# Kernel tuning notes

Hardware: AMD Instinct MI355X
Metric: run time of the kernel (lower is better)

The kernel has to match this reference:

```python
import jax, jax.numpy as jnp
import numpy as np

B, T, C = 4, 2048, 1024
H = 16
D = C // H  # head_dim = 64


def setup_inputs() -> dict:
    key = jax.random.key(0)
    ks = jax.random.split(key, 9)
    s = 1.0 / np.sqrt(C)
    return {
        "x": jax.random.normal(ks[0], (B, T, C), dtype=jnp.float32),
        "Wk": jax.random.uniform(ks[1], (C, C), jnp.float32, -s, s),
        "bk": jax.random.uniform(ks[2], (C,), jnp.float32, -s, s),
        "Wq": jax.random.uniform(ks[3], (C, C), jnp.float32, -s, s),
        "bq": jax.random.uniform(ks[4], (C,), jnp.float32, -s, s),
        "Wv": jax.random.uniform(ks[5], (C, C), jnp.float32, -s, s),
        "bv": jax.random.uniform(ks[6], (C,), jnp.float32, -s, s),
        "Wp": jax.random.uniform(ks[7], (C, C), jnp.float32, -s, s),
        "bp": jax.random.uniform(ks[8], (C,), jnp.float32, -s, s),
    }


def reference(x, Wk, bk, Wq, bq, Wv, bv, Wp, bp):
    # projections -> (B, H, T, D)
    def split_heads(y):
        return y.reshape(B, T, H, D).transpose(0, 2, 1, 3)

    k = split_heads(x @ Wk.T + bk)
    q = split_heads(x @ Wq.T + bq)
    v = split_heads(x @ Wv.T + bv)

    att = jnp.einsum("bhtd,bhsd->bhts", q, k) / np.sqrt(D).astype(np.float32)
    causal = jnp.tril(jnp.ones((T, T), dtype=bool))
    att = jnp.where(causal, att, -jnp.inf)
    att = jax.nn.softmax(att, axis=-1)

    y = jnp.einsum("bhts,bhsd->bhtd", att, v)  # (B,H,T,D)
    y = y.transpose(0, 2, 1, 3).reshape(B, T, C)
    return y @ Wp.T + bp
```

## Files before the change

kernel.cpp:

```cpp
#include <hip/hip_runtime.h>
#include <hip/hip_bf16.h>

typedef unsigned short u16;
typedef unsigned int u32;
typedef short short8 __attribute__((ext_vector_type(8)));
typedef short short4v __attribute__((ext_vector_type(4)));
typedef float f32x4 __attribute__((ext_vector_type(4)));

#define MFMA16(a, b, c) __builtin_amdgcn_mfma_f32_16x16x32_bf16((a), (b), (c), 0, 0, 0)

constexpr int kB = 4, kT = 2048, kC = 1024, kH = 16, kD = 64;
constexpr int kBT = kB * kT;
constexpr long kQKV = (long)kB * kH * kT * kD;
constexpr float kSC = 0.125f * 1.4426950408889634f;

__device__ inline u16 f2bf(float f) {
    __hip_bfloat16 h = __float2bfloat16(f);
    return *reinterpret_cast<u16*>(&h);
}
__device__ inline u32 pkbf_trunc(float lo, float hi) {
    u32 a = __builtin_bit_cast(u32, lo);
    u32 b = __builtin_bit_cast(u32, hi);
    return (b & 0xFFFF0000u) | (a >> 16);
}
__device__ inline u32 pkbf_rne(float lo, float hi) {
    return ((u32)f2bf(hi) << 16) | (u32)f2bf(lo);
}

__device__ inline void cp16(const u16* g, u16* l) {
    __builtin_amdgcn_global_load_lds(
        (const __attribute__((address_space(1))) unsigned int*)g,
        (__attribute__((address_space(3))) unsigned int*)l, 16, 0, 0);
}

__global__ __launch_bounds__(256) void cast_kernel(
    const float* __restrict__ x,  const float* __restrict__ Wk,
    const float* __restrict__ Wq, const float* __restrict__ Wv,
    const float* __restrict__ Wp,
    u16* __restrict__ xb, u16* __restrict__ wkb, u16* __restrict__ wqb,
    u16* __restrict__ wvb, u16* __restrict__ wpb)
{
    const long id = (long)blockIdx.x * 256 + threadIdx.x;
    const float* src;
    u16* dst;
    long off;
    if (id < 2097152) {
        src = x; dst = xb; off = id;
    } else {
        const long w = (id - 2097152) >> 18;
        off = (id - 2097152) & 262143;
        src = (w == 0) ? Wk : (w == 1) ? Wq : (w == 2) ? Wv : Wp;
        dst = (w == 0) ? wkb : (w == 1) ? wqb : (w == 2) ? wvb : wpb;
    }
    f32x4 v = *(const f32x4*)&src[off * 4];
    short4v s = {(short)f2bf(v[0]), (short)f2bf(v[1]),
                 (short)f2bf(v[2]), (short)f2bf(v[3])};
    *(short4v*)&dst[off * 4] = s;
}

__global__ __launch_bounds__(256) void qkv_gemm_bf16(
    const u16* __restrict__ xb,
    const u16* __restrict__ wkb, const u16* __restrict__ wqb,
    const u16* __restrict__ wvb,
    const float* __restrict__ bk, const float* __restrict__ bq,
    const float* __restrict__ bv,
    u16* __restrict__ kw, u16* __restrict__ qw, u16* __restrict__ vw)
{
    __shared__ u16 As[128 * 32];
    __shared__ u16 Bs[128 * 32];
    const int tid = threadIdx.x;
    const int lane = tid & 63;
    const int wid = tid >> 6;
    const int l15 = lane & 15;
    const int quad = lane >> 4;
    const int m0 = blockIdx.x * 128;
    const int n0 = blockIdx.y * 128;
    const int z = blockIdx.z;

    const u16* W = (z == 0) ? wkb : (z == 1) ? wqb : wvb;
    const float* bias = (z == 0) ? bk : (z == 1) ? bq : bv;

    f32x4 zero = {0.f, 0.f, 0.f, 0.f};
    f32x4 acc[4][4];
#pragma unroll
    for (int i = 0; i < 4; ++i)
#pragma unroll
        for (int j = 0; j < 4; ++j) acc[i][j] = zero;

    const int wm = (wid & 1) * 64;
    const int wn = (wid >> 1) * 64;

    const int sRow = tid >> 2;
    const int sCol = (tid & 3) * 8;
    const int ldsOff = sRow * 32 + sCol;

    for (int k0 = 0; k0 < kC; k0 += 32) {
        cp16(&xb[(long)(m0 + sRow) * kC + k0 + sCol],      &As[ldsOff]);
        cp16(&xb[(long)(m0 + 64 + sRow) * kC + k0 + sCol], &As[64 * 32 + ldsOff]);
        cp16(&W[(long)(n0 + sRow) * kC + k0 + sCol],       &Bs[ldsOff]);
        cp16(&W[(long)(n0 + 64 + sRow) * kC + k0 + sCol],  &Bs[64 * 32 + ldsOff]);
        __syncthreads();
        short8 af[4], bfr[4];
#pragma unroll
        for (int mt = 0; mt < 4; ++mt)
            af[mt] = *(const short8*)&As[(wm + mt * 16 + l15) * 32 + quad * 8];
#pragma unroll
        for (int nt = 0; nt < 4; ++nt)
            bfr[nt] = *(const short8*)&Bs[(wn + nt * 16 + l15) * 32 + quad * 8];
#pragma unroll
        for (int mt = 0; mt < 4; ++mt)
#pragma unroll
            for (int nt = 0; nt < 4; ++nt)
                acc[mt][nt] = MFMA16(af[mt], bfr[nt], acc[mt][nt]);
        __syncthreads();
    }

    const float scale = (z == 1) ? kSC : 1.0f;
#pragma unroll
    for (int nt = 0; nt < 4; ++nt) {
        const int n = n0 + wn + nt * 16 + l15;
        const float bias_f = bias[n];
        const int h = n >> 6, d = n & 63;
#pragma unroll
        for (int mt = 0; mt < 4; ++mt) {
#pragma unroll
            for (int r = 0; r < 4; ++r) {
                const int m = m0 + wm + mt * 16 + quad * 4 + r;
                const int b = m >> 11, t = m & 2047;
                const float v = (acc[mt][nt][r] + bias_f) * scale;
                const int bh = b * kH + h;
                if (z == 2) {
                    vw[((long)bh * kD + d) * kT + t] = f2bf(v);
                } else {
                    u16* dst = (z == 0) ? kw : qw;
                    dst[((long)bh * kT + t) * kD + d] = f2bf(v);
                }
            }
        }
    }
}

__global__ __launch_bounds__(256) void qkv_gemm_kernel(
    const float* __restrict__ x,
    const float* __restrict__ Wk, const float* __restrict__ bk,
    const float* __restrict__ Wq, const float* __restrict__ bq,
    const float* __restrict__ Wv, const float* __restrict__ bv,
    u16* __restrict__ kw, u16* __restrict__ qw, u16* __restrict__ vw)
{
    __shared__ u16 As[128 * 32];
    __shared__ u16 Bs[128 * 32];
    const int tid = threadIdx.x;
    const int lane = tid & 63;
    const int wid = tid >> 6;
    const int l15 = lane & 15;
    const int quad = lane >> 4;
    const int m0 = blockIdx.x * 128;
    const int n0 = blockIdx.y * 128;
    const int z = blockIdx.z;

    const float* W = (z == 0) ? Wk : (z == 1) ? Wq : Wv;
    const float* bias = (z == 0) ? bk : (z == 1) ? bq : bv;

    f32x4 zero = {0.f, 0.f, 0.f, 0.f};
    f32x4 acc[4][4];
#pragma unroll
    for (int i = 0; i < 4; ++i)
#pragma unroll
        for (int j = 0; j < 4; ++j) acc[i][j] = zero;

    const int wm = (wid & 1) * 64;
    const int wn = (wid >> 1) * 64;
    const int row4 = tid >> 3;
    const int col4 = (tid & 7) * 4;

    for (int k0 = 0; k0 < kC; k0 += 32) {
#pragma unroll
        for (int p = 0; p < 4; ++p) {
            const int r = p * 32 + row4;
            f32x4 xa = *(const f32x4*)&x[(long)(m0 + r) * kC + k0 + col4];
            f32x4 wa = *(const f32x4*)&W[(long)(n0 + r) * kC + k0 + col4];
            short4v xs = {(short)f2bf(xa[0]), (short)f2bf(xa[1]),
                          (short)f2bf(xa[2]), (short)f2bf(xa[3])};
            short4v wsv = {(short)f2bf(wa[0]), (short)f2bf(wa[1]),
                           (short)f2bf(wa[2]), (short)f2bf(wa[3])};
            *(short4v*)&As[r * 32 + col4] = xs;
            *(short4v*)&Bs[r * 32 + col4] = wsv;
        }
        __syncthreads();
        short8 af[4], bfr[4];
#pragma unroll
        for (int mt = 0; mt < 4; ++mt)
            af[mt] = *(const short8*)&As[(wm + mt * 16 + l15) * 32 + quad * 8];
#pragma unroll
        for (int nt = 0; nt < 4; ++nt)
            bfr[nt] = *(const short8*)&Bs[(wn + nt * 16 + l15) * 32 + quad * 8];
#pragma unroll
        for (int mt = 0; mt < 4; ++mt)
#pragma unroll
            for (int nt = 0; nt < 4; ++nt)
                acc[mt][nt] = MFMA16(af[mt], bfr[nt], acc[mt][nt]);
        __syncthreads();
    }

    const float scale = (z == 1) ? kSC : 1.0f;
#pragma unroll
    for (int nt = 0; nt < 4; ++nt) {
        const int n = n0 + wn + nt * 16 + l15;
        const float bias_f = bias[n];
        const int h = n >> 6, d = n & 63;
#pragma unroll
        for (int mt = 0; mt < 4; ++mt) {
#pragma unroll
            for (int r = 0; r < 4; ++r) {
                const int m = m0 + wm + mt * 16 + quad * 4 + r;
                const int b = m >> 11, t = m & 2047;
                const float v = (acc[mt][nt][r] + bias_f) * scale;
                const int bh = b * kH + h;
                if (z == 2) {
                    vw[((long)bh * kD + d) * kT + t] = f2bf(v);
                } else {
                    u16* dst = (z == 0) ? kw : qw;
                    dst[((long)bh * kT + t) * kD + d] = f2bf(v);
                }
            }
        }
    }
}

__global__ __launch_bounds__(256) void attn_kernel(
    const u16* qw, const u16* kw, const u16* vw, u16* ow)
{
    __shared__ u16 Ks[64 * 72];
    __shared__ u16 VT[64 * 72];
    __shared__ u16 Pb[64 * 72];

    const int tid = threadIdx.x;
    const int lane = tid & 63;
    const int wid = tid >> 6;
    const int l15 = lane & 15;
    const int quad = lane >> 4;
    const int id = blockIdx.x;
    const int bh = id & 63;
    const int pr = id >> 6;

    const float NEG = -1.0e30f;
    f32x4 zero = {0.f, 0.f, 0.f, 0.f};

    const int r0 = tid >> 3;
    const int c0 = (tid & 7) * 8;
    const int r1 = r0 + 32;

    const u16* kbase = kw + (long)bh * kT * kD;
    const u16* vbase = vw + (long)bh * kD * kT;

#pragma unroll
    for (int ph = 0; ph < 2; ++ph) {
        const int qt64 = ph ? (31 - pr) : pr;
        const int t_base = qt64 * 64;
        const int tw = t_base + wid * 16;

        short8 qf0, qf1;
        {
            const u16* qp = qw + ((long)bh * kT + tw + l15) * kD;
            qf0 = *(const short8*)&qp[quad * 8];
            qf1 = *(const short8*)&qp[32 + quad * 8];
        }

        f32x4 oacc[4];
#pragma unroll
        for (int mo = 0; mo < 4; ++mo) oacc[mo] = zero;
        float l_acc = 0.f;

        const u16* kp0 = kbase + (long)r0 * kD + c0;
        const u16* kp1 = kbase + (long)r1 * kD + c0;
        const u16* vp0 = vbase + (long)r0 * kT + c0;
        const u16* vp1 = vbase + (long)r1 * kT + c0;
        short8 ka = *(const short8*)kp0;
        short8 kb = *(const short8*)kp1;
        short8 va = *(const short8*)vp0;
        short8 vb = *(const short8*)vp1;
        kp0 += 64 * kD; kp1 += 64 * kD;
        vp0 += 64;      vp1 += 64;

        const int n_st = qt64 + 1;
        for (int st = 0; st < n_st; ++st) {
            *(short8*)&Ks[r0 * 72 + c0] = ka;
            *(short8*)&Ks[r1 * 72 + c0] = kb;
            *(short8*)&VT[r0 * 72 + c0] = va;
            *(short8*)&VT[r1 * 72 + c0] = vb;
            __syncthreads();
            if (st + 1 < n_st) {
                ka = *(const short8*)kp0;
                kb = *(const short8*)kp1;
                va = *(const short8*)vp0;
                vb = *(const short8*)vp1;
                kp0 += 64 * kD; kp1 += 64 * kD;
                vp0 += 64;      vp1 += 64;
            }

            short8 kf[4][2];
#pragma unroll
            for (int ms = 0; ms < 4; ++ms)
#pragma unroll
                for (int k2 = 0; k2 < 2; ++k2)
                    kf[ms][k2] = *(const short8*)&Ks[(ms * 16 + l15) * 72 + k2 * 32 + quad * 8];
            f32x4 sacc[4];
#pragma unroll
            for (int ms = 0; ms < 4; ++ms) {
                sacc[ms] = MFMA16(kf[ms][0], qf0, zero);
                sacc[ms] = MFMA16(kf[ms][1], qf1, sacc[ms]);
            }

            if (st == n_st - 1) {
                const int tl = wid * 16 + l15;
#pragma unroll
                for (int ms = 0; ms < 4; ++ms)
#pragma unroll
                    for (int r = 0; r < 4; ++r)
                        if (ms * 16 + quad * 4 + r > tl) sacc[ms][r] = NEG;
            }

            float rs = 0.f;
#pragma unroll
            for (int ms = 0; ms < 4; ++ms)
#pragma unroll
                for (int r = 0; r < 4; ++r) {
                    const float p = exp2f(sacc[ms][r]);
                    sacc[ms][r] = p;
                    rs += p;
                }
            rs += __shfl_xor(rs, 16);
            rs += __shfl_xor(rs, 32);
            l_acc += rs;

#pragma unroll
            for (int ms = 0; ms < 4; ++ms) {
                uint2 pk;
                pk.x = pkbf_trunc(sacc[ms][0], sacc[ms][1]);
                pk.y = pkbf_trunc(sacc[ms][2], sacc[ms][3]);
                *(uint2*)&Pb[(wid * 16 + l15) * 72 + ms * 16 + quad * 4] = pk;
            }

            short8 vf[4][2];
#pragma unroll
            for (int mo = 0; mo < 4; ++mo)
#pragma unroll
                for (int k2 = 0; k2 < 2; ++k2)
                    vf[mo][k2] = *(const short8*)&VT[(mo * 16 + l15) * 72 + k2 * 32 + quad * 8];
            short8 pf0 = *(const short8*)&Pb[(wid * 16 + l15) * 72 + quad * 8];
            short8 pf1 = *(const short8*)&Pb[(wid * 16 + l15) * 72 + 32 + quad * 8];
#pragma unroll
            for (int mo = 0; mo < 4; ++mo) {
                oacc[mo] = MFMA16(vf[mo][0], pf0, oacc[mo]);
                oacc[mo] = MFMA16(vf[mo][1], pf1, oacc[mo]);
            }
            __syncthreads();
        }

        const float inv = 1.0f / l_acc;
        const int t = tw + l15;
        u16* op = ow + ((long)bh * kT + t) * kD;
#pragma unroll
        for (int mo = 0; mo < 4; ++mo) {
            uint2 ov;
            ov.x = pkbf_rne(oacc[mo][0] * inv, oacc[mo][1] * inv);
            ov.y = pkbf_rne(oacc[mo][2] * inv, oacc[mo][3] * inv);
            *(uint2*)&op[mo * 16 + quad * 4] = ov;
        }
    }
}

__global__ __launch_bounds__(256) void out_gemm_bf16(
    const u16* __restrict__ ob, const u16* __restrict__ wpb,
    const float* __restrict__ bp, float* __restrict__ out)
{
    __shared__ u16 As[128 * 32];
    __shared__ u16 Bs[128 * 32];
    const int tid = threadIdx.x;
    const int lane = tid & 63;
    const int wid = tid >> 6;
    const int l15 = lane & 15;
    const int quad = lane >> 4;
    const int m0 = blockIdx.x * 128;
    const int n0 = blockIdx.y * 128;

    f32x4 zero = {0.f, 0.f, 0.f, 0.f};
    f32x4 acc[4][4];
#pragma unroll
    for (int i = 0; i < 4; ++i)
#pragma unroll
        for (int j = 0; j < 4; ++j) acc[i][j] = zero;

    const int wm = (wid & 1) * 64;
    const int wn = (wid >> 1) * 64;

    const int sRow = tid >> 2;
    const int sCol = (tid & 3) * 8;
    const int ldsOff = sRow * 32 + sCol;

    for (int k0 = 0; k0 < kC; k0 += 32) {
        const int h = k0 >> 6;
        const int d = (k0 & 63) + sCol;
        {
            const int m = m0 + sRow, b = m >> 11, t = m & 2047;
            cp16(&ob[(((long)b * kH + h) * kT + t) * kD + d], &As[ldsOff]);
        }
        {
            const int m = m0 + 64 + sRow, b = m >> 11, t = m & 2047;
            cp16(&ob[(((long)b * kH + h) * kT + t) * kD + d], &As[64 * 32 + ldsOff]);
        }
        cp16(&wpb[(long)(n0 + sRow) * kC + k0 + sCol],      &Bs[ldsOff]);
        cp16(&wpb[(long)(n0 + 64 + sRow) * kC + k0 + sCol], &Bs[64 * 32 + ldsOff]);
        __syncthreads();
        short8 af[4], bfr[4];
#pragma unroll
        for (int mt = 0; mt < 4; ++mt)
            af[mt] = *(const short8*)&As[(wm + mt * 16 + l15) * 32 + quad * 8];
#pragma unroll
        for (int nt = 0; nt < 4; ++nt)
            bfr[nt] = *(const short8*)&Bs[(wn + nt * 16 + l15) * 32 + quad * 8];
#pragma unroll
        for (int mt = 0; mt < 4; ++mt)
#pragma unroll
            for (int nt = 0; nt < 4; ++nt)
                acc[mt][nt] = MFMA16(af[mt], bfr[nt], acc[mt][nt]);
        __syncthreads();
    }

#pragma unroll
    for (int nt = 0; nt < 4; ++nt) {
        const int n = n0 + wn + nt * 16 + l15;
        const float bias_f = bp[n];
#pragma unroll
        for (int mt = 0; mt < 4; ++mt) {
#pragma unroll
            for (int r = 0; r < 4; ++r) {
                const int m = m0 + wm + mt * 16 + quad * 4 + r;
                out[(long)m * kC + n] = acc[mt][nt][r] + bias_f;
            }
        }
    }
}

__global__ __launch_bounds__(256) void out_gemm_kernel(
    const u16* __restrict__ ow, const float* __restrict__ Wp,
    const float* __restrict__ bp, float* __restrict__ out)
{
    __shared__ u16 As[128 * 32];
    __shared__ u16 Bs[128 * 32];
    const int tid = threadIdx.x;
    const int lane = tid & 63;
    const int wid = tid >> 6;
    const int l15 = lane & 15;
    const int quad = lane >> 4;
    const int m0 = blockIdx.x * 128;
    const int n0 = blockIdx.y * 128;

    f32x4 zero = {0.f, 0.f, 0.f, 0.f};
    f32x4 acc[4][4];
#pragma unroll
    for (int i = 0; i < 4; ++i)
#pragma unroll
        for (int j = 0; j < 4; ++j) acc[i][j] = zero;

    const int wm = (wid & 1) * 64;
    const int wn = (wid >> 1) * 64;

    const int r0 = tid >> 2;
    const int kkA = (tid & 3) * 8;
    const int r1 = r0 + 64;
    const int row4 = tid >> 3;
    const int col4 = (tid & 7) * 4;

    for (int k0 = 0; k0 < kC; k0 += 32) {
        {
            const int m = m0 + r0, b = m >> 11, t = m & 2047;
            const int kk = k0 + kkA, h = kk >> 6, d = kk & 63;
            *(short8*)&As[r0 * 32 + kkA] =
                *(const short8*)&ow[(((long)b * kH + h) * kT + t) * kD + d];
        }
        {
            const int m = m0 + r1, b = m >> 11, t = m & 2047;
            const int kk = k0 + kkA, h = kk >> 6, d = kk & 63;
            *(short8*)&As[r1 * 32 + kkA] =
                *(const short8*)&ow[(((long)b * kH + h) * kT + t) * kD + d];
        }
#pragma unroll
        for (int p = 0; p < 4; ++p) {
            const int r = p * 32 + row4;
            f32x4 wa = *(const f32x4*)&Wp[(long)(n0 + r) * kC + k0 + col4];
            short4v wsv = {(short)f2bf(wa[0]), (short)f2bf(wa[1]),
                           (short)f2bf(wa[2]), (short)f2bf(wa[3])};
            *(short4v*)&Bs[r * 32 + col4] = wsv;
        }
        __syncthreads();
        short8 af[4], bfr[4];
#pragma unroll
        for (int mt = 0; mt < 4; ++mt)
            af[mt] = *(const short8*)&As[(wm + mt * 16 + l15) * 32 + quad * 8];
#pragma unroll
        for (int nt = 0; nt < 4; ++nt)
            bfr[nt] = *(const short8*)&Bs[(wn + nt * 16 + l15) * 32 + quad * 8];
#pragma unroll
        for (int mt = 0; mt < 4; ++mt)
#pragma unroll
            for (int nt = 0; nt < 4; ++nt)
                acc[mt][nt] = MFMA16(af[mt], bfr[nt], acc[mt][nt]);
        __syncthreads();
    }

#pragma unroll
    for (int nt = 0; nt < 4; ++nt) {
        const int n = n0 + wn + nt * 16 + l15;
        const float bias_f = bp[n];
#pragma unroll
        for (int mt = 0; mt < 4; ++mt) {
#pragma unroll
            for (int r = 0; r < 4; ++r) {
                const int m = m0 + wm + mt * 16 + quad * 4 + r;
                out[(long)m * kC + n] = acc[mt][nt][r] + bias_f;
            }
        }
    }
}

extern "C" void kernel_launch(void* const* d_in, const int* in_sizes, int n_in,
                              void* d_out, int out_size, void* d_ws, size_t ws_size,
                              hipStream_t stream) {
    const float* x  = (const float*)d_in[0];
    const float* Wk = (const float*)d_in[1];
    const float* bk = (const float*)d_in[2];
    const float* Wq = (const float*)d_in[3];
    const float* bq = (const float*)d_in[4];
    const float* Wv = (const float*)d_in[5];
    const float* bv = (const float*)d_in[6];
    const float* Wp = (const float*)d_in[7];
    const float* bp = (const float*)d_in[8];
    float* out = (float*)d_out;

    u16* ws = (u16*)d_ws;
    const size_t kNeed = 72ull * 1024 * 1024;

    if (ws_size >= kNeed) {
        u16* k_ws = ws;
        u16* q_ws = ws + kQKV;
        u16* v_ws = ws + 2 * kQKV;
        u16* xb   = ws + 3 * kQKV;
        u16* o_ws = xb;
        u16* wkb  = ws + 4 * kQKV;
        u16* wqb  = wkb + (long)kC * kC;
        u16* wvb  = wqb + (long)kC * kC;
        u16* wpb  = wvb + (long)kC * kC;

        cast_kernel<<<12288, 256, 0, stream>>>(x, Wk, Wq, Wv, Wp,
                                               xb, wkb, wqb, wvb, wpb);
        qkv_gemm_bf16<<<dim3(kBT / 128, kC / 128, 3), 256, 0, stream>>>(
            xb, wkb, wqb, wvb, bk, bq, bv, k_ws, q_ws, v_ws);
        attn_kernel<<<1024, 256, 0, stream>>>(q_ws, k_ws, v_ws, o_ws);
        out_gemm_bf16<<<dim3(kBT / 128, kC / 128), 256, 0, stream>>>(
            o_ws, wpb, bp, out);
    } else {
        u16* k_ws = ws;
        u16* q_ws = ws + kQKV;
        u16* v_ws = ws + 2 * kQKV;
        u16* o_ws = q_ws;

        qkv_gemm_kernel<<<dim3(kBT / 128, kC / 128, 3), 256, 0, stream>>>(
            x, Wk, bk, Wq, bq, Wv, bv, k_ws, q_ws, v_ws);
        attn_kernel<<<1024, 256, 0, stream>>>(q_ws, k_ws, v_ws, o_ws);
        out_gemm_kernel<<<dim3(kBT / 128, kC / 128), 256, 0, stream>>>(
            o_ws, Wp, bp, out);
    }
}
```

Baseline: 281.6 us.

## Double-buffer K/V tiles in attention, swizzle LDS, compute row sums via MFMA

The attention kernel now keeps two LDS buffers for K and V tiles, so the next tile is written while the current one is consumed and one barrier per iteration is removed. The padded layout is replaced by an XOR swizzle on 8-element chunks to avoid bank conflicts without padding. Softmax row sums are taken from an extra MFMA against a ones vector instead of scalar adds and cross-lane shuffles, and the bf16 truncation pack uses a byte-permute. The extra MFMAs and the larger LDS footprint may lower occupancy, and the sum now comes from the bf16-rounded probabilities.

```diff
diff --git a/kernel.cpp b/kernel.cpp
--- a/kernel.cpp
+++ b/kernel.cpp
@@ -19,9 +19,8 @@
     return *reinterpret_cast<u16*>(&h);
 }
 __device__ inline u32 pkbf_trunc(float lo, float hi) {
-    u32 a = __builtin_bit_cast(u32, lo);
-    u32 b = __builtin_bit_cast(u32, hi);
-    return (b & 0xFFFF0000u) | (a >> 16);
+    return __builtin_amdgcn_perm(__builtin_bit_cast(u32, hi),
+                                 __builtin_bit_cast(u32, lo), 0x07060302u);
 }
 __device__ inline u32 pkbf_rne(float lo, float hi) {
     return ((u32)f2bf(hi) << 16) | (u32)f2bf(lo);
@@ -230,9 +229,9 @@
 __global__ __launch_bounds__(256) void attn_kernel(
     const u16* qw, const u16* kw, const u16* vw, u16* ow)
 {
-    __shared__ u16 Ks[64 * 72];
-    __shared__ u16 VT[64 * 72];
-    __shared__ u16 Pb[64 * 72];
+    __shared__ u16 Ks[2][64 * 64];
+    __shared__ u16 VT[2][64 * 64];
+    __shared__ u16 Pb[64 * 64];
 
     const int tid = threadIdx.x;
     const int lane = tid & 63;
@@ -245,10 +244,17 @@
 
     const float NEG = -1.0e30f;
     f32x4 zero = {0.f, 0.f, 0.f, 0.f};
+    const short8 onesf = {(short)0x3F80, (short)0x3F80, (short)0x3F80, (short)0x3F80,
+                          (short)0x3F80, (short)0x3F80, (short)0x3F80, (short)0x3F80};
 
     const int r0 = tid >> 3;
-    const int c0 = (tid & 7) * 8;
+    const int cc = tid & 7;
     const int r1 = r0 + 32;
+    const int sw0 = r0 * 64 + ((cc ^ (r0 & 7)) * 8);
+    const int sw1 = r1 * 64 + ((cc ^ (r1 & 7)) * 8);
+    const int c0e = cc * 8;
+
+    const int rl7 = l15 & 7;
 
     const u16* kbase = kw + (long)bh * kT * kD;
     const u16* vbase = vw + (long)bh * kD * kT;
@@ -256,8 +262,7 @@
 #pragma unroll
     for (int ph = 0; ph < 2; ++ph) {
         const int qt64 = ph ? (31 - pr) : pr;
-        const int t_base = qt64 * 64;
-        const int tw = t_base + wid * 16;
+        const int tw = qt64 * 64 + wid * 16;
 
         short8 qf0, qf1;
         {
@@ -269,27 +274,45 @@
         f32x4 oacc[4];
 #pragma unroll
         for (int mo = 0; mo < 4; ++mo) oacc[mo] = zero;
-        float l_acc = 0.f;
-
-        const u16* kp0 = kbase + (long)r0 * kD + c0;
-        const u16* kp1 = kbase + (long)r1 * kD + c0;
-        const u16* vp0 = vbase + (long)r0 * kT + c0;
-        const u16* vp1 = vbase + (long)r1 * kT + c0;
+        f32x4 lsum = zero;
+
+        const int n_st = qt64 + 1;
+
+        const u16* kp0 = kbase + (long)r0 * kD + c0e;
+        const u16* kp1 = kbase + (long)r1 * kD + c0e;
+        const u16* vp0 = vbase + (long)r0 * kT + c0e;
+        const u16* vp1 = vbase + (long)r1 * kT + c0e;
         short8 ka = *(const short8*)kp0;
         short8 kb = *(const short8*)kp1;
         short8 va = *(const short8*)vp0;
         short8 vb = *(const short8*)vp1;
         kp0 += 64 * kD; kp1 += 64 * kD;
         vp0 += 64;      vp1 += 64;
-
-        const int n_st = qt64 + 1;
+        __syncthreads();
+        *(short8*)&Ks[0][sw0] = ka;
+        *(short8*)&Ks[0][sw1] = kb;
+        *(short8*)&VT[0][sw0] = va;
+        *(short8*)&VT[0][sw1] = vb;
+        if (n_st > 1) {
+            ka = *(const short8*)kp0;
+            kb = *(const short8*)kp1;
+            va = *(const short8*)vp0;
+            vb = *(const short8*)vp1;
+            kp0 += 64 * kD; kp1 += 64 * kD;
+            vp0 += 64;      vp1 += 64;
+        }
+
         for (int st = 0; st < n_st; ++st) {
-            *(short8*)&Ks[r0 * 72 + c0] = ka;
-            *(short8*)&Ks[r1 * 72 + c0] = kb;
-            *(short8*)&VT[r0 * 72 + c0] = va;
-            *(short8*)&VT[r1 * 72 + c0] = vb;
             __syncthreads();
+            const int cur = st & 1;
             if (st + 1 < n_st) {
+                const int nxt = cur ^ 1;
+                *(short8*)&Ks[nxt][sw0] = ka;
+                *(short8*)&Ks[nxt][sw1] = kb;
+                *(short8*)&VT[nxt][sw0] = va;
+                *(short8*)&VT[nxt][sw1] = vb;
+            }
+            if (st + 2 < n_st) {
                 ka = *(const short8*)kp0;
                 kb = *(const short8*)kp1;
                 va = *(const short8*)vp0;
@@ -300,10 +323,13 @@
 
             short8 kf[4][2];
 #pragma unroll
-            for (int ms = 0; ms < 4; ++ms)
+            for (int ms = 0; ms < 4; ++ms) {
+                const int row = ms * 16 + l15;
 #pragma unroll
                 for (int k2 = 0; k2 < 2; ++k2)
-                    kf[ms][k2] = *(const short8*)&Ks[(ms * 16 + l15) * 72 + k2 * 32 + quad * 8];
+                    kf[ms][k2] = *(const short8*)
+                        &Ks[cur][row * 64 + (((k2 * 4 + quad) ^ rl7) * 8)];
+            }
             f32x4 sacc[4];
 #pragma unroll
             for (int ms = 0; ms < 4; ++ms) {
@@ -320,44 +346,37 @@
                         if (ms * 16 + quad * 4 + r > tl) sacc[ms][r] = NEG;
             }
 
-            float rs = 0.f;
-#pragma unroll
-            for (int ms = 0; ms < 4; ++ms)
-#pragma unroll
-                for (int r = 0; r < 4; ++r) {
-                    const float p = exp2f(sacc[ms][r]);
-                    sacc[ms][r] = p;
-                    rs += p;
-                }
-            rs += __shfl_xor(rs, 16);
-            rs += __shfl_xor(rs, 32);
-            l_acc += rs;
-
+            const int prow = wid * 16 + l15;
 #pragma unroll
             for (int ms = 0; ms < 4; ++ms) {
+                const float p0 = exp2f(sacc[ms][0]);
+                const float p1 = exp2f(sacc[ms][1]);
+                const float p2 = exp2f(sacc[ms][2]);
+                const float p3 = exp2f(sacc[ms][3]);
                 uint2 pk;
-                pk.x = pkbf_trunc(sacc[ms][0], sacc[ms][1]);
-                pk.y = pkbf_trunc(sacc[ms][2], sacc[ms][3]);
-                *(uint2*)&Pb[(wid * 16 + l15) * 72 + ms * 16 + quad * 4] = pk;
-            }
-
-            short8 vf[4][2];
-#pragma unroll
-            for (int mo = 0; mo < 4; ++mo)
-#pragma unroll
-                for (int k2 = 0; k2 < 2; ++k2)
-                    vf[mo][k2] = *(const short8*)&VT[(mo * 16 + l15) * 72 + k2 * 32 + quad * 8];
-            short8 pf0 = *(const short8*)&Pb[(wid * 16 + l15) * 72 + quad * 8];
-            short8 pf1 = *(const short8*)&Pb[(wid * 16 + l15) * 72 + 32 + quad * 8];
+                pk.x = pkbf_trunc(p0, p1);
+                pk.y = pkbf_trunc(p2, p3);
+                const int chunk = (ms * 2 + (quad >> 1)) ^ rl7;
+                *(uint2*)&Pb[prow * 64 + chunk * 8 + (quad & 1) * 4] = pk;
+            }
+
+            short8 pf0 = *(const short8*)&Pb[prow * 64 + ((quad ^ rl7) * 8)];
+            short8 pf1 = *(const short8*)&Pb[prow * 64 + (((4 + quad) ^ rl7) * 8)];
+            lsum = MFMA16(onesf, pf0, lsum);
+            lsum = MFMA16(onesf, pf1, lsum);
 #pragma unroll
             for (int mo = 0; mo < 4; ++mo) {
-                oacc[mo] = MFMA16(vf[mo][0], pf0, oacc[mo]);
-                oacc[mo] = MFMA16(vf[mo][1], pf1, oacc[mo]);
-            }
-            __syncthreads();
-        }
-
-        const float inv = 1.0f / l_acc;
+                const int row = mo * 16 + l15;
+                short8 vf0 = *(const short8*)
+                    &VT[cur][row * 64 + ((quad ^ rl7) * 8)];
+                short8 vf1 = *(const short8*)
+                    &VT[cur][row * 64 + (((4 + quad) ^ rl7) * 8)];
+                oacc[mo] = MFMA16(vf0, pf0, oacc[mo]);
+                oacc[mo] = MFMA16(vf1, pf1, oacc[mo]);
+            }
+        }
+
+        const float inv = 1.0f / lsum[0];
         const int t = tw + l15;
         u16* op = ow + ((long)bh * kT + t) * kD;
 #pragma unroll
```

After: 280.6 us. Within noise of the previous version (-0.4%).
